# Kernel optimization log

Hardware: AMD Instinct MI355X
Metric: run time of the kernel (lower is better)

The kernel has to match this reference:

```python
import jax, jax.numpy as jnp
import numpy as np

H, D = 12, 64  # num_heads, head_dim (embed_size=768)


def setup_inputs() -> dict:
    key = jax.random.key(0)
    k1, k2, k3 = jax.random.split(key, 3)
    z = jax.random.normal(k1, (2, 2048, 768), dtype=jnp.float32)
    W = jax.random.normal(k2, (768, 3 * H * D), dtype=jnp.float32) * (768 ** -0.5)
    bias = jax.random.normal(k3, (3 * H * D,), dtype=jnp.float32) * 0.02
    return {"z": z, "W": W, "bias": bias}


def reference(z, W, bias):
    b, n, _ = z.shape
    # fused QKV projection, reshaped exactly as torch: (b, n, h, d, 3)
    kvq = (z @ W + bias).reshape(b, n, H, D, 3)
    k = kvq[..., 0]  # (b, n, h, d)
    v = kvq[..., 1]
    q = kvq[..., 2]
    qk = jnp.einsum("bqhd,bkhd->bhqk", q, k)  # full O(n^2) scores
    # NOTE: original module scales AFTER softmax (faithful reproduction of bug)
    a = jax.nn.softmax(qk, axis=-1) * (D ** -0.5)
    sa = jnp.einsum("bhqk,bkhd->bqhd", a, v)
    return sa.reshape(b, n, H * D)
```

## Files before the change

kernel.cpp:

```cpp
#include <hip/hip_runtime.h>
#include <hip/hip_bf16.h>
#include <math.h>

#define BB 2
#define NN 2048
#define HH 12
#define DD 64
#define EE 768
#define FF 2304

typedef __attribute__((ext_vector_type(8))) _Float16 f16x8;
typedef __attribute__((ext_vector_type(4))) short bf16x4;
typedef __attribute__((ext_vector_type(4))) float f32x4;
typedef __attribute__((address_space(3))) unsigned int lds_u32;
typedef const __attribute__((address_space(1))) unsigned int glb_u32;

static __device__ __forceinline__ ushort f2bf(float x) {
    __hip_bfloat16 h = __float2bfloat16(x);
    return *reinterpret_cast<ushort*>(&h);
}
static __device__ __forceinline__ float bf2f(ushort u) {
    unsigned int v = ((unsigned int)u) << 16;
    float f;
    __builtin_memcpy(&f, &v, 4);
    return f;
}

__global__ __launch_bounds__(256) void convert_z(
    const float* __restrict__ z, _Float16* __restrict__ Zf)
{
    const int i = (blockIdx.x * 256 + threadIdx.x) * 8;
    const float4 a = *(const float4*)&z[i];
    const float4 b = *(const float4*)&z[i + 4];
    const float v[8] = {a.x, a.y, a.z, a.w, b.x, b.y, b.z, b.w};
    f16x8 h8;
#pragma unroll
    for (int j = 0; j < 8; ++j) h8[j] = (_Float16)v[j];
    *(f16x8*)&Zf[i] = h8;
}

__global__ __launch_bounds__(256) void convert_w(
    const float* __restrict__ W, _Float16* __restrict__ Wtf)
{
    __shared__ float T[64][65];
    const int t  = threadIdx.x;
    const int c0 = blockIdx.x * 64;
    const int k0 = blockIdx.y * 64;
#pragma unroll
    for (int i = 0; i < 4; ++i) {
        const int row = i * 16 + (t >> 4);
        const int c4  = (t & 15) * 4;
        const float4 w4 = *(const float4*)&W[(size_t)(k0 + row) * FF + c0 + c4];
        T[row][c4 + 0] = w4.x; T[row][c4 + 1] = w4.y;
        T[row][c4 + 2] = w4.z; T[row][c4 + 3] = w4.w;
    }
    __syncthreads();
#pragma unroll
    for (int u = 0; u < 2; ++u) {
        const int id = t + u * 256;
        const int c  = id >> 3;
        const int kc = id & 7;
        f16x8 h8;
#pragma unroll
        for (int j = 0; j < 8; ++j) h8[j] = (_Float16)T[kc * 8 + j][c];
        *(f16x8*)&Wtf[(size_t)(c0 + c) * EE + k0 + kc * 8] = h8;
    }
}

__global__ __launch_bounds__(256, 2) void qkv_gemm(
    const _Float16* __restrict__ Zf, const _Float16* __restrict__ Wtf,
    const float* __restrict__ bias,
    _Float16* __restrict__ Qf, _Float16* __restrict__ Kf,
    ushort* __restrict__ Vtb)
{
    __shared__ __align__(16) _Float16 As[128 * 32];
    __shared__ __align__(16) _Float16 Bs[128 * 32];

    const int tid  = threadIdx.x;
    const int wave = tid >> 6;
    const int lane = tid & 63;
    const int l4   = lane & 15;
    const int quad = lane >> 4;
    const int wx   = wave & 1;
    const int wy   = wave >> 1;
    const int row0 = blockIdx.y * 128;
    const int col0 = blockIdx.x * 128;

    int offAB[2], ldsoff[2];
#pragma unroll
    for (int u = 0; u < 2; ++u) {
        const int g = tid + u * 256;
        offAB[u]  = (g >> 2) * EE + (g & 3) * 8;
        ldsoff[u] = (u * 256 + wave * 64) * 16;
    }
    const _Float16* ZB = Zf  + (size_t)row0 * EE;
    const _Float16* WB = Wtf + (size_t)col0 * EE;

    f32x4 acc[4][4];
#pragma unroll
    for (int mi = 0; mi < 4; ++mi)
#pragma unroll
        for (int ni = 0; ni < 4; ++ni) acc[mi][ni] = (f32x4){0.f, 0.f, 0.f, 0.f};

    for (int k0 = 0; k0 < EE; k0 += 32) {
#pragma unroll
        for (int u = 0; u < 2; ++u) {
            __builtin_amdgcn_global_load_lds((glb_u32*)(ZB + offAB[u] + k0),
                                             (lds_u32*)((char*)As + ldsoff[u]), 16, 0, 0);
            __builtin_amdgcn_global_load_lds((glb_u32*)(WB + offAB[u] + k0),
                                             (lds_u32*)((char*)Bs + ldsoff[u]), 16, 0, 0);
        }
        __syncthreads();

        f16x8 aF[4], bF[4];
#pragma unroll
        for (int mi = 0; mi < 4; ++mi)
            aF[mi] = *(const f16x8*)&As[(wy * 64 + mi * 16 + l4) * 32 + quad * 8];
#pragma unroll
        for (int ni = 0; ni < 4; ++ni)
            bF[ni] = *(const f16x8*)&Bs[(wx * 64 + ni * 16 + l4) * 32 + quad * 8];
#pragma unroll
        for (int mi = 0; mi < 4; ++mi)
#pragma unroll
            for (int ni = 0; ni < 4; ++ni)
                acc[mi][ni] = __builtin_amdgcn_mfma_f32_16x16x32_f16(
                    aF[mi], bF[ni], acc[mi][ni], 0, 0, 0);
        __syncthreads();
    }

#pragma unroll
    for (int ni = 0; ni < 4; ++ni) {
        const int col = col0 + wx * 64 + ni * 16 + l4;
        const int h   = col / 192;
        const int rem = col - h * 192;
        const int d   = rem / 3;
        const int t3  = rem - d * 3;
        const float bv = bias[col];
#pragma unroll
        for (int mi = 0; mi < 4; ++mi) {
#pragma unroll
            for (int r = 0; r < 4; ++r) {
                const int grow = row0 + wy * 64 + mi * 16 + quad * 4 + r;
                const int bb = grow >> 11;
                const int q  = grow & 2047;
                const float val = acc[mi][ni][r] + bv;
                if (t3 == 0) {
                    Kf[((size_t)(bb * HH + h) * NN + q) * DD + d] = (_Float16)val;
                } else if (t3 == 1) {
                    Vtb[((size_t)(bb * HH + h) * DD + d) * NN + q] = f2bf(val);
                } else {
                    Qf[((size_t)(bb * HH + h) * NN + q) * DD + d] = (_Float16)val;
                }
            }
        }
    }
}

__global__ __launch_bounds__(256, 3) void attn_kernel(
    const _Float16* __restrict__ Kf, const ushort* __restrict__ Vtb,
    const _Float16* __restrict__ Qf, float* __restrict__ out)
{
    __shared__ __align__(16) _Float16 KS[2][4096];
    __shared__ __align__(16) ushort   VS[2][4096];
    __shared__ float lRed[2][2][16];

    const int tid  = threadIdx.x;
    const int wave = tid >> 6;
    const int lane = tid & 63;
    const int l4   = lane & 15;
    const int quad = lane >> 4;
    const int ky   = wave >> 1;
    const int qx   = wave & 1;
    const int h  = blockIdx.y;
    const int bb = blockIdx.z;
    const int bh = bb * HH + h;
    const int q0 = blockIdx.x * 64;

    f16x8 qF[2][2];
#pragma unroll
    for (int qc = 0; qc < 2; ++qc) {
        const _Float16* qb = Qf + ((size_t)bh * NN + q0 + qx * 32 + qc * 16 + l4) * DD + quad * 8;
        qF[qc][0] = *(const f16x8*)qb;
        qF[qc][1] = *(const f16x8*)(qb + 32);
    }

    f32x4 O[4][2];
#pragma unroll
    for (int dt = 0; dt < 4; ++dt)
#pragma unroll
        for (int qc = 0; qc < 2; ++qc) O[dt][qc] = (f32x4){0.f, 0.f, 0.f, 0.f};
    float lp[2] = {0.f, 0.f};

    const _Float16* KB = Kf  + (size_t)bh * NN * DD;
    const ushort*   VB = Vtb + (size_t)bh * DD * NN;

    int rowg[2], c16g[2], di[2];
#pragma unroll
    for (int u = 0; u < 2; ++u) {
        const int g = tid + u * 256;
        rowg[u] = g >> 3;
        c16g[u] = g & 7;
        di[u]   = rowg[u] * 64 + ((c16g[u] ^ (rowg[u] & 7)) * 8);
    }

    uint4 kr[2], vr[2];
#pragma unroll
    for (int u = 0; u < 2; ++u) {
        kr[u] = *(const uint4*)(KB + (size_t)rowg[u] * DD + c16g[u] * 8);
        vr[u] = *(const uint4*)(VB + (size_t)rowg[u] * NN + c16g[u] * 8);
    }
#pragma unroll
    for (int u = 0; u < 2; ++u) {
        *(uint4*)&KS[0][di[u]] = kr[u];
        *(uint4*)&VS[0][di[u]] = vr[u];
    }
    __syncthreads();

    for (int kt = 0; kt < 32; ++kt) {
        const int cur = kt & 1;
        if (kt < 31) {
            const int k0n = (kt + 1) * 64;
#pragma unroll
            for (int u = 0; u < 2; ++u) {
                kr[u] = *(const uint4*)(KB + (size_t)(k0n + rowg[u]) * DD + c16g[u] * 8);
                vr[u] = *(const uint4*)(VB + (size_t)rowg[u] * NN + k0n + c16g[u] * 8);
            }
        }

        f16x8 kF[2][2];
#pragma unroll
        for (int kc = 0; kc < 2; ++kc) {
            const int row = ky * 32 + kc * 16 + l4;
            const int r7  = row & 7;
            const int base = row * 64;
            kF[kc][0] = *(const f16x8*)&KS[cur][base + (((quad    ) ^ r7) * 8)];
            kF[kc][1] = *(const f16x8*)&KS[cur][base + (((quad + 4) ^ r7) * 8)];
        }
        bf16x4 vF[4][2];
#pragma unroll
        for (int dt = 0; dt < 4; ++dt) {
            const int d  = dt * 16 + l4;
            const int r7 = d & 7;
            const int base = d * 64;
#pragma unroll
            for (int kc = 0; kc < 2; ++kc) {
                const int g = ky * 4 + kc * 2 + (quad >> 1);
                vF[dt][kc] = *(const bf16x4*)&VS[cur][base + ((g ^ r7) * 8) + (quad & 1) * 4];
            }
        }

        bf16x4 pF[2][2];
#pragma unroll
        for (int kc = 0; kc < 2; ++kc)
#pragma unroll
            for (int qc = 0; qc < 2; ++qc) {
                f32x4 s = {0.f, 0.f, 0.f, 0.f};
                s = __builtin_amdgcn_mfma_f32_16x16x32_f16(kF[kc][0], qF[qc][0], s, 0, 0, 0);
                s = __builtin_amdgcn_mfma_f32_16x16x32_f16(kF[kc][1], qF[qc][1], s, 0, 0, 0);
#pragma unroll
                for (int r = 0; r < 4; ++r) {
                    const ushort b = f2bf(__expf(s[r]));
                    pF[kc][qc][r] = (short)b;
                    lp[qc] += bf2f(b);
                }
            }

#pragma unroll
        for (int dt = 0; dt < 4; ++dt)
#pragma unroll
            for (int qc = 0; qc < 2; ++qc) {
                f32x4 o = O[dt][qc];
                o = __builtin_amdgcn_mfma_f32_16x16x16bf16_1k(vF[dt][0], pF[0][qc], o, 0, 0, 0);
                o = __builtin_amdgcn_mfma_f32_16x16x16bf16_1k(vF[dt][1], pF[1][qc], o, 0, 0, 0);
                O[dt][qc] = o;
            }

        if (kt < 31) {
            const int nxt = 1 - cur;
#pragma unroll
            for (int u = 0; u < 2; ++u) {
                *(uint4*)&KS[nxt][di[u]] = kr[u];
                *(uint4*)&VS[nxt][di[u]] = vr[u];
            }
        }
        __syncthreads();
    }

#pragma unroll
    for (int qc = 0; qc < 2; ++qc) {
        lp[qc] += __shfl_xor(lp[qc], 16);
        lp[qc] += __shfl_xor(lp[qc], 32);
    }

    f32x4* RedV = (f32x4*)&VS[0][0];
    if (ky == 1) {
#pragma unroll
        for (int dt = 0; dt < 4; ++dt)
#pragma unroll
            for (int qc = 0; qc < 2; ++qc)
                RedV[(dt * 2 + qc) * 128 + qx * 64 + lane] = O[dt][qc];
        if (lane < 16) {
            lRed[qx][0][lane] = lp[0];
            lRed[qx][1][lane] = lp[1];
        }
    }
    __syncthreads();
    if (ky == 0) {
        float inv[2];
#pragma unroll
        for (int qc = 0; qc < 2; ++qc)
            inv[qc] = 0.125f / (lp[qc] + lRed[qx][qc][l4]);
#pragma unroll
        for (int dt = 0; dt < 4; ++dt) {
#pragma unroll
            for (int qc = 0; qc < 2; ++qc) {
                const f32x4 o2 = RedV[(dt * 2 + qc) * 128 + qx * 64 + lane];
                const int q = q0 + qx * 32 + qc * 16 + l4;
                float4 ov;
                ov.x = (O[dt][qc][0] + o2[0]) * inv[qc];
                ov.y = (O[dt][qc][1] + o2[1]) * inv[qc];
                ov.z = (O[dt][qc][2] + o2[2]) * inv[qc];
                ov.w = (O[dt][qc][3] + o2[3]) * inv[qc];
                *(float4*)&out[((size_t)(bb * NN + q)) * (HH * DD) + h * DD + dt * 16 + quad * 4] = ov;
            }
        }
    }
}

extern "C" void kernel_launch(void* const* d_in, const int* in_sizes, int n_in,
                              void* d_out, int out_size, void* d_ws, size_t ws_size,
                              hipStream_t stream)
{
    const float* z    = (const float*)d_in[0];
    const float* W    = (const float*)d_in[1];
    const float* bias = (const float*)d_in[2];
    float* out = (float*)d_out;

    const size_t N1 = (size_t)BB * HH * NN * DD;
    const size_t NW = (size_t)EE * FF;
    _Float16* ws  = (_Float16*)d_ws;
    _Float16* Zf  = ws;
    _Float16* Wtf = ws + N1;
    _Float16* Qf  = ws + N1 + NW;
    _Float16* Kf  = ws + 2 * N1 + NW;
    ushort*   Vtb = (ushort*)(ws + 3 * N1 + NW);

    convert_z<<<dim3(1536), 256, 0, stream>>>(z, Zf);
    convert_w<<<dim3(36, 12), 256, 0, stream>>>(W, Wtf);
    qkv_gemm<<<dim3(18, 32), 256, 0, stream>>>(Zf, Wtf, bias, Qf, Kf, Vtb);
    attn_kernel<<<dim3(32, 12, 2), 256, 0, stream>>>(Kf, Vtb, Qf, out);
}
```

Baseline: 166.2 us.

## Drop LDS staging in attention, split keys across waves; double GEMM K-tile

The attention kernel no longer stages K/V tiles in shared memory with block-wide barriers. Each wave now loads its own 16-key slice of K and V straight from global memory into registers, prefetches the next slice, and processes all 64 queries of the block, with a three-way LDS reduction at the end. The grid becomes (bh, qblock) so consecutive blocks share a head's K/V in cache. The QKV GEMM doubles its K-step to 64 to halve the number of barriers per tile. This trades LDS traffic and syncs for narrower, less coalesced global loads and more registers per thread.

Result: slower. 181.3 us (+9.1%).

```diff
diff --git a/kernel.cpp b/kernel.cpp
--- a/kernel.cpp
+++ b/kernel.cpp
@@ -73,8 +73,8 @@
     _Float16* __restrict__ Qf, _Float16* __restrict__ Kf,
     ushort* __restrict__ Vtb)
 {
-    __shared__ __align__(16) _Float16 As[128 * 32];
-    __shared__ __align__(16) _Float16 Bs[128 * 32];
+    __shared__ __align__(16) _Float16 As[128 * 64];
+    __shared__ __align__(16) _Float16 Bs[128 * 64];
 
     const int tid  = threadIdx.x;
     const int wave = tid >> 6;
@@ -86,11 +86,11 @@
     const int row0 = blockIdx.y * 128;
     const int col0 = blockIdx.x * 128;
 
-    int offAB[2], ldsoff[2];
-#pragma unroll
-    for (int u = 0; u < 2; ++u) {
+    int offAB[4], ldsoff[4];
+#pragma unroll
+    for (int u = 0; u < 4; ++u) {
         const int g = tid + u * 256;
-        offAB[u]  = (g >> 2) * EE + (g & 3) * 8;
+        offAB[u]  = (g >> 3) * EE + (g & 7) * 8;
         ldsoff[u] = (u * 256 + wave * 64) * 16;
     }
     const _Float16* ZB = Zf  + (size_t)row0 * EE;
@@ -102,9 +102,9 @@
 #pragma unroll
         for (int ni = 0; ni < 4; ++ni) acc[mi][ni] = (f32x4){0.f, 0.f, 0.f, 0.f};
 
-    for (int k0 = 0; k0 < EE; k0 += 32) {
-#pragma unroll
-        for (int u = 0; u < 2; ++u) {
+    for (int k0 = 0; k0 < EE; k0 += 64) {
+#pragma unroll
+        for (int u = 0; u < 4; ++u) {
             __builtin_amdgcn_global_load_lds((glb_u32*)(ZB + offAB[u] + k0),
                                              (lds_u32*)((char*)As + ldsoff[u]), 16, 0, 0);
             __builtin_amdgcn_global_load_lds((glb_u32*)(WB + offAB[u] + k0),
@@ -112,19 +112,22 @@
         }
         __syncthreads();
 
-        f16x8 aF[4], bF[4];
-#pragma unroll
-        for (int mi = 0; mi < 4; ++mi)
-            aF[mi] = *(const f16x8*)&As[(wy * 64 + mi * 16 + l4) * 32 + quad * 8];
-#pragma unroll
-        for (int ni = 0; ni < 4; ++ni)
-            bF[ni] = *(const f16x8*)&Bs[(wx * 64 + ni * 16 + l4) * 32 + quad * 8];
-#pragma unroll
-        for (int mi = 0; mi < 4; ++mi)
+#pragma unroll
+        for (int ks = 0; ks < 2; ++ks) {
+            f16x8 aF[4], bF[4];
+#pragma unroll
+            for (int mi = 0; mi < 4; ++mi)
+                aF[mi] = *(const f16x8*)&As[(wy * 64 + mi * 16 + l4) * 64 + ks * 32 + quad * 8];
 #pragma unroll
             for (int ni = 0; ni < 4; ++ni)
-                acc[mi][ni] = __builtin_amdgcn_mfma_f32_16x16x32_f16(
-                    aF[mi], bF[ni], acc[mi][ni], 0, 0, 0);
+                bF[ni] = *(const f16x8*)&Bs[(wx * 64 + ni * 16 + l4) * 64 + ks * 32 + quad * 8];
+#pragma unroll
+            for (int mi = 0; mi < 4; ++mi)
+#pragma unroll
+                for (int ni = 0; ni < 4; ++ni)
+                    acc[mi][ni] = __builtin_amdgcn_mfma_f32_16x16x32_f16(
+                        aF[mi], bF[ni], acc[mi][ni], 0, 0, 0);
+        }
         __syncthreads();
     }
 
@@ -160,168 +163,129 @@
     const _Float16* __restrict__ Kf, const ushort* __restrict__ Vtb,
     const _Float16* __restrict__ Qf, float* __restrict__ out)
 {
-    __shared__ __align__(16) _Float16 KS[2][4096];
-    __shared__ __align__(16) ushort   VS[2][4096];
-    __shared__ float lRed[2][2][16];
+    __shared__ __align__(16) float Red[3 * 16 * 64 * 4];
+    __shared__ float lRed[3][4][16];
 
     const int tid  = threadIdx.x;
     const int wave = tid >> 6;
     const int lane = tid & 63;
     const int l4   = lane & 15;
     const int quad = lane >> 4;
-    const int ky   = wave >> 1;
-    const int qx   = wave & 1;
-    const int h  = blockIdx.y;
-    const int bb = blockIdx.z;
-    const int bh = bb * HH + h;
-    const int q0 = blockIdx.x * 64;
-
-    f16x8 qF[2][2];
-#pragma unroll
-    for (int qc = 0; qc < 2; ++qc) {
-        const _Float16* qb = Qf + ((size_t)bh * NN + q0 + qx * 32 + qc * 16 + l4) * DD + quad * 8;
+    const int bh   = blockIdx.x;
+    const int q0   = blockIdx.y * 64;
+
+    const _Float16* QB = Qf  + (size_t)bh * NN * DD;
+    const _Float16* KB = Kf  + (size_t)bh * NN * DD;
+    const ushort*   VB = Vtb + (size_t)bh * DD * NN;
+
+    f16x8 qF[4][2];
+#pragma unroll
+    for (int qc = 0; qc < 4; ++qc) {
+        const _Float16* qb = QB + (size_t)(q0 + qc * 16 + l4) * DD + quad * 8;
         qF[qc][0] = *(const f16x8*)qb;
         qF[qc][1] = *(const f16x8*)(qb + 32);
     }
 
-    f32x4 O[4][2];
+    f32x4 O[4][4];
 #pragma unroll
     for (int dt = 0; dt < 4; ++dt)
 #pragma unroll
-        for (int qc = 0; qc < 2; ++qc) O[dt][qc] = (f32x4){0.f, 0.f, 0.f, 0.f};
-    float lp[2] = {0.f, 0.f};
-
-    const _Float16* KB = Kf  + (size_t)bh * NN * DD;
-    const ushort*   VB = Vtb + (size_t)bh * DD * NN;
-
-    int rowg[2], c16g[2], di[2];
-#pragma unroll
-    for (int u = 0; u < 2; ++u) {
-        const int g = tid + u * 256;
-        rowg[u] = g >> 3;
-        c16g[u] = g & 7;
-        di[u]   = rowg[u] * 64 + ((c16g[u] ^ (rowg[u] & 7)) * 8);
-    }
-
-    uint4 kr[2], vr[2];
-#pragma unroll
-    for (int u = 0; u < 2; ++u) {
-        kr[u] = *(const uint4*)(KB + (size_t)rowg[u] * DD + c16g[u] * 8);
-        vr[u] = *(const uint4*)(VB + (size_t)rowg[u] * NN + c16g[u] * 8);
-    }
-#pragma unroll
-    for (int u = 0; u < 2; ++u) {
-        *(uint4*)&KS[0][di[u]] = kr[u];
-        *(uint4*)&VS[0][di[u]] = vr[u];
-    }
-    __syncthreads();
-
-    for (int kt = 0; kt < 32; ++kt) {
-        const int cur = kt & 1;
-        if (kt < 31) {
-            const int k0n = (kt + 1) * 64;
-#pragma unroll
-            for (int u = 0; u < 2; ++u) {
-                kr[u] = *(const uint4*)(KB + (size_t)(k0n + rowg[u]) * DD + c16g[u] * 8);
-                vr[u] = *(const uint4*)(VB + (size_t)rowg[u] * NN + k0n + c16g[u] * 8);
+        for (int qc = 0; qc < 4; ++qc) O[dt][qc] = (f32x4){0.f, 0.f, 0.f, 0.f};
+    float lp[4] = {0.f, 0.f, 0.f, 0.f};
+
+    int kb = wave * 16;
+    f16x8 kc0 = *(const f16x8*)(KB + (size_t)(kb + l4) * DD + quad * 8);
+    f16x8 kc1 = *(const f16x8*)(KB + (size_t)(kb + l4) * DD + 32 + quad * 8);
+    bf16x4 vc[4];
+#pragma unroll
+    for (int dt = 0; dt < 4; ++dt)
+        vc[dt] = *(const bf16x4*)(VB + (size_t)(dt * 16 + l4) * NN + kb + quad * 4);
+
+    for (int it = 0; it < 32; ++it) {
+        f16x8 kn0, kn1;
+        bf16x4 vn[4];
+        if (it < 31) {
+            const int kn = kb + 64;
+            kn0 = *(const f16x8*)(KB + (size_t)(kn + l4) * DD + quad * 8);
+            kn1 = *(const f16x8*)(KB + (size_t)(kn + l4) * DD + 32 + quad * 8);
+#pragma unroll
+            for (int dt = 0; dt < 4; ++dt)
+                vn[dt] = *(const bf16x4*)(VB + (size_t)(dt * 16 + l4) * NN + kn + quad * 4);
+        }
+
+        bf16x4 pF[4];
+#pragma unroll
+        for (int qc = 0; qc < 4; ++qc) {
+            f32x4 s = {0.f, 0.f, 0.f, 0.f};
+            s = __builtin_amdgcn_mfma_f32_16x16x32_f16(kc0, qF[qc][0], s, 0, 0, 0);
+            s = __builtin_amdgcn_mfma_f32_16x16x32_f16(kc1, qF[qc][1], s, 0, 0, 0);
+#pragma unroll
+            for (int r = 0; r < 4; ++r) {
+                const ushort b = f2bf(__expf(s[r]));
+                pF[qc][r] = (short)b;
+                lp[qc] += bf2f(b);
             }
         }
 
-        f16x8 kF[2][2];
-#pragma unroll
-        for (int kc = 0; kc < 2; ++kc) {
-            const int row = ky * 32 + kc * 16 + l4;
-            const int r7  = row & 7;
-            const int base = row * 64;
-            kF[kc][0] = *(const f16x8*)&KS[cur][base + (((quad    ) ^ r7) * 8)];
-            kF[kc][1] = *(const f16x8*)&KS[cur][base + (((quad + 4) ^ r7) * 8)];
-        }
-        bf16x4 vF[4][2];
-#pragma unroll
-        for (int dt = 0; dt < 4; ++dt) {
-            const int d  = dt * 16 + l4;
-            const int r7 = d & 7;
-            const int base = d * 64;
-#pragma unroll
-            for (int kc = 0; kc < 2; ++kc) {
-                const int g = ky * 4 + kc * 2 + (quad >> 1);
-                vF[dt][kc] = *(const bf16x4*)&VS[cur][base + ((g ^ r7) * 8) + (quad & 1) * 4];
-            }
-        }
-
-        bf16x4 pF[2][2];
-#pragma unroll
-        for (int kc = 0; kc < 2; ++kc)
-#pragma unroll
-            for (int qc = 0; qc < 2; ++qc) {
-                f32x4 s = {0.f, 0.f, 0.f, 0.f};
-                s = __builtin_amdgcn_mfma_f32_16x16x32_f16(kF[kc][0], qF[qc][0], s, 0, 0, 0);
-                s = __builtin_amdgcn_mfma_f32_16x16x32_f16(kF[kc][1], qF[qc][1], s, 0, 0, 0);
-#pragma unroll
-                for (int r = 0; r < 4; ++r) {
-                    const ushort b = f2bf(__expf(s[r]));
-                    pF[kc][qc][r] = (short)b;
-                    lp[qc] += bf2f(b);
-                }
-            }
-
 #pragma unroll
         for (int dt = 0; dt < 4; ++dt)
 #pragma unroll
-            for (int qc = 0; qc < 2; ++qc) {
-                f32x4 o = O[dt][qc];
-                o = __builtin_amdgcn_mfma_f32_16x16x16bf16_1k(vF[dt][0], pF[0][qc], o, 0, 0, 0);
-                o = __builtin_amdgcn_mfma_f32_16x16x16bf16_1k(vF[dt][1], pF[1][qc], o, 0, 0, 0);
-                O[dt][qc] = o;
-            }
-
-        if (kt < 31) {
-            const int nxt = 1 - cur;
-#pragma unroll
-            for (int u = 0; u < 2; ++u) {
-                *(uint4*)&KS[nxt][di[u]] = kr[u];
-                *(uint4*)&VS[nxt][di[u]] = vr[u];
-            }
-        }
-        __syncthreads();
-    }
-
-#pragma unroll
-    for (int qc = 0; qc < 2; ++qc) {
+            for (int qc = 0; qc < 4; ++qc)
+                O[dt][qc] = __builtin_amdgcn_mfma_f32_16x16x16bf16_1k(
+                    vc[dt], pF[qc], O[dt][qc], 0, 0, 0);
+
+        if (it < 31) {
+            kc0 = kn0; kc1 = kn1;
+#pragma unroll
+            for (int dt = 0; dt < 4; ++dt) vc[dt] = vn[dt];
+        }
+        kb += 64;
+    }
+
+#pragma unroll
+    for (int qc = 0; qc < 4; ++qc) {
         lp[qc] += __shfl_xor(lp[qc], 16);
         lp[qc] += __shfl_xor(lp[qc], 32);
     }
 
-    f32x4* RedV = (f32x4*)&VS[0][0];
-    if (ky == 1) {
+    f32x4* RedV = (f32x4*)Red;
+    if (wave > 0) {
+        const int wb = (wave - 1) * 16 * 64;
 #pragma unroll
         for (int dt = 0; dt < 4; ++dt)
 #pragma unroll
-            for (int qc = 0; qc < 2; ++qc)
-                RedV[(dt * 2 + qc) * 128 + qx * 64 + lane] = O[dt][qc];
+            for (int qc = 0; qc < 4; ++qc)
+                RedV[wb + (dt * 4 + qc) * 64 + lane] = O[dt][qc];
         if (lane < 16) {
-            lRed[qx][0][lane] = lp[0];
-            lRed[qx][1][lane] = lp[1];
+#pragma unroll
+            for (int qc = 0; qc < 4; ++qc) lRed[wave - 1][qc][lane] = lp[qc];
         }
     }
     __syncthreads();
-    if (ky == 0) {
-        float inv[2];
-#pragma unroll
-        for (int qc = 0; qc < 2; ++qc)
-            inv[qc] = 0.125f / (lp[qc] + lRed[qx][qc][l4]);
+    if (wave == 0) {
+        const int bb = bh / HH;
+        const int h  = bh - bb * HH;
+        float inv[4];
+#pragma unroll
+        for (int qc = 0; qc < 4; ++qc)
+            inv[qc] = 0.125f /
+                (lp[qc] + lRed[0][qc][l4] + lRed[1][qc][l4] + lRed[2][qc][l4]);
 #pragma unroll
         for (int dt = 0; dt < 4; ++dt) {
 #pragma unroll
-            for (int qc = 0; qc < 2; ++qc) {
-                const f32x4 o2 = RedV[(dt * 2 + qc) * 128 + qx * 64 + lane];
-                const int q = q0 + qx * 32 + qc * 16 + l4;
+            for (int qc = 0; qc < 4; ++qc) {
+                f32x4 o = O[dt][qc];
+#pragma unroll
+                for (int w = 0; w < 3; ++w) {
+                    const f32x4 o2 = RedV[w * 16 * 64 + (dt * 4 + qc) * 64 + lane];
+                    o[0] += o2[0]; o[1] += o2[1]; o[2] += o2[2]; o[3] += o2[3];
+                }
+                const int q = q0 + qc * 16 + l4;
                 float4 ov;
-                ov.x = (O[dt][qc][0] + o2[0]) * inv[qc];
-                ov.y = (O[dt][qc][1] + o2[1]) * inv[qc];
-                ov.z = (O[dt][qc][2] + o2[2]) * inv[qc];
-                ov.w = (O[dt][qc][3] + o2[3]) * inv[qc];
-                *(float4*)&out[((size_t)(bb * NN + q)) * (HH * DD) + h * DD + dt * 16 + quad * 4] = ov;
+                ov.x = o[0] * inv[qc]; ov.y = o[1] * inv[qc];
+                ov.z = o[2] * inv[qc]; ov.w = o[3] * inv[qc];
+                *(float4*)&out[((size_t)(bb * NN + q)) * (HH * DD) + h * DD +
+                               dt * 16 + quad * 4] = ov;
             }
         }
     }
@@ -348,5 +312,5 @@
     convert_z<<<dim3(1536), 256, 0, stream>>>(z, Zf);
     convert_w<<<dim3(36, 12), 256, 0, stream>>>(W, Wtf);
     qkv_gemm<<<dim3(18, 32), 256, 0, stream>>>(Zf, Wtf, bias, Qf, Kf, Vtb);
-    attn_kernel<<<dim3(32, 12, 2), 256, 0, stream>>>(Kf, Vtb, Qf, out);
-}
+    attn_kernel<<<dim3(24, 32), 256, 0, stream>>>(Kf, Vtb, Qf, out);
+}
```
